# Optimization experiments

Measured on AMD Instinct MI355X. Metric: run time of the kernel, lower is better.

Reference implementation:

```python
import jax, jax.numpy as jnp
import numpy as np

N_GRID = 65160   # 181*360 lat-lon grid nodes (= self.size)
N_MESH = 40962   # level-6 icosphere nodes
N_TOT = N_GRID + N_MESH
E = 521280
IN_CH = 96
HID = 256
OUT_CH = 96


def setup_inputs() -> dict:
    key = jax.random.key(0)
    ks = jax.random.split(key, 12)
    inp = {
        'x': jax.random.normal(ks[0], (1, IN_CH, N_MESH), jnp.float32),
        'x_res_grid': jax.random.normal(ks[1], (1, IN_CH, N_GRID), jnp.float32),
        'edge_index': jax.random.randint(ks[2], (2, E), 0, N_TOT, jnp.int64),
        # GCNConv 1 (in_ch -> 256), glorot-ish scale
        'W1': jax.random.normal(ks[3], (IN_CH, HID), jnp.float32) * (2.0 / (IN_CH + HID)) ** 0.5,
        'b1': jnp.zeros((HID,), jnp.float32),
        # GCNConv 2 (256 -> 256)
        'W2': jax.random.normal(ks[4], (HID, HID), jnp.float32) * (2.0 / (HID + HID)) ** 0.5,
        'b2': jnp.zeros((HID,), jnp.float32),
        # Lmodel2: Linear(256,256) -> Linear(256,out_ch), xavier_normal
        'Wl1': jax.random.normal(ks[5], (HID, HID), jnp.float32) * (2.0 / (HID + HID)) ** 0.5,
        'bl1': jnp.zeros((HID,), jnp.float32),
        'Wl2': jax.random.normal(ks[6], (HID, OUT_CH), jnp.float32) * (2.0 / (HID + OUT_CH)) ** 0.5,
        'bl2': jnp.zeros((OUT_CH,), jnp.float32),
    }
    return inp


def _gcn_norm(edge_index, n_nodes):
    # PyG gcn_norm with add_self_loops=True, edge_weight=1
    loop = jnp.arange(n_nodes, dtype=edge_index.dtype)
    src = jnp.concatenate([edge_index[0], loop])
    dst = jnp.concatenate([edge_index[1], loop])
    deg = jnp.zeros((n_nodes,), jnp.float32).at[dst].add(1.0)
    dinv = jnp.where(deg > 0, jax.lax.rsqrt(deg), 0.0)
    norm = dinv[src] * dinv[dst]  # [E+N]
    return src, dst, norm


def _gcn_conv(h, W, b, src, dst, norm):
    # h: [B, N, C] -> [B, N, H]; x' = D^-1/2 (A+I) D^-1/2 (h W) + b
    m = h @ W                                   # [B, N, H]
    msg = m[:, src, :] * norm[None, :, None]    # [B, E+N, H]
    agg = jnp.zeros(m.shape, m.dtype).at[:, dst].add(msg)
    return agg + b


def reference(x, x_res_grid, edge_index, W1, b1, W2, b2, Wl1, bl1, Wl2, bl2):
    nodes = jnp.concatenate([x_res_grid, x], axis=-1)  # [B, C, N]
    h = nodes.transpose(0, 2, 1)                       # [B, N, C]
    n = h.shape[1]
    src, dst, norm = _gcn_norm(edge_index, n)
    h = _gcn_conv(h, W1, b1, src, dst, norm)
    h = jax.nn.gelu(h, approximate=False)              # torch nn.GELU (exact erf)
    h = _gcn_conv(h, W2, b2, src, dst, norm)           # [B, N, 256]
    g = h[:, :N_GRID, :]                               # slice grid nodes
    out = (g @ Wl1 + bl1) @ Wl2 + bl2                  # [B, size, out_ch]
    return out.transpose(0, 2, 1)                      # [B, out_ch, size]
```

## Files before the change

### kernel.cpp

```cpp
#include <hip/hip_runtime.h>
#include <math.h>

#define N_GRID 65160
#define N_MESH 40962
#define N_TOT  106122
#define NE     521280
#define IN_CH  96
#define HID    256
#define OUT_CH 96

typedef __attribute__((ext_vector_type(8))) short bf16x8;
typedef __attribute__((ext_vector_type(4))) float f32x4;

__device__ __forceinline__ unsigned short f2bf(float f) {
  unsigned u = __float_as_uint(f);
  return (unsigned short)((u + 0x7FFFu + ((u >> 16) & 1u)) >> 16);
}
__device__ __forceinline__ float bf2f(unsigned short s) {
  return __uint_as_float(((unsigned)s) << 16);
}
__device__ __forceinline__ float4 ldbf4(const unsigned short* p) {
  ushort4 u = *(const ushort4*)p;
  return make_float4(bf2f(u.x), bf2f(u.y), bf2f(u.z), bf2f(u.w));
}

__global__ void k_concat_transpose(const float* __restrict__ xg, const float* __restrict__ xm,
                                   unsigned short* __restrict__ h) {
  __shared__ float tile[IN_CH][65];
  int base = blockIdx.x * 64;
  int t = threadIdx.x;
#pragma unroll
  for (int it = 0; it < 24; ++it) {
    int lin = t + it * 256;
    int c  = lin >> 6;
    int n0 = lin & 63;
    int n = base + n0;
    float v = 0.f;
    if (n < N_TOT) {
      v = (n < N_GRID) ? xg[(size_t)c * N_GRID + n]
                       : xm[(size_t)c * N_MESH + (n - N_GRID)];
    }
    tile[c][n0] = v;
  }
  __syncthreads();
#pragma unroll
  for (int it = 0; it < 24; ++it) {
    int lin = t + it * 256;
    int c  = lin % 96;
    int n0 = lin / 96;
    int n = base + n0;
    if (n < N_TOT) h[(size_t)n * IN_CH + c] = f2bf(tile[c][n0]);
  }
}

__global__ void k_transpose_out(const float* __restrict__ tb, float* __restrict__ out) {
  __shared__ float tile[IN_CH][65];
  int base = blockIdx.x * 64;
  int t = threadIdx.x;
#pragma unroll
  for (int it = 0; it < 24; ++it) {
    int lin = t + it * 256;
    int c  = lin % 96;
    int n0 = lin / 96;
    int n = base + n0;
    if (n < N_GRID) tile[c][n0] = tb[(size_t)n * 96 + c];
  }
  __syncthreads();
#pragma unroll
  for (int it = 0; it < 24; ++it) {
    int lin = t + it * 256;
    int c  = lin >> 6;
    int n0 = lin & 63;
    int n = base + n0;
    if (n < N_GRID) out[(size_t)c * N_GRID + n] = tile[c][n0];
  }
}

__global__ void k_zeroi(int* __restrict__ p, int n) {
  int i = blockIdx.x * 256 + threadIdx.x;
  if (i < n) p[i] = 0;
}
__global__ void k_seti(int* __restrict__ p, int v) { *p = v; }

__global__ void k_hist(const int* __restrict__ dst, int* __restrict__ deg) {
  int e = blockIdx.x * 256 + threadIdx.x;
  if (e < NE) atomicAdd(&deg[dst[e]], 1);
}

__global__ void k_blocksum(const int* __restrict__ deg, int* __restrict__ bsum, int n) {
  __shared__ int s[256];
  int i = blockIdx.x * 256 + threadIdx.x;
  s[threadIdx.x] = (i < n) ? deg[i] : 0;
  __syncthreads();
  for (int st = 128; st > 0; st >>= 1) {
    if (threadIdx.x < st) s[threadIdx.x] += s[threadIdx.x + st];
    __syncthreads();
  }
  if (threadIdx.x == 0) bsum[blockIdx.x] = s[0];
}

__global__ void k_scanbsum(int* __restrict__ bsum, int nb) {
  __shared__ int s[512];
  int t = threadIdx.x;
  int v = (t < nb) ? bsum[t] : 0;
  s[t] = v;
  __syncthreads();
  for (int off = 1; off < 512; off <<= 1) {
    int x = (t >= off) ? s[t - off] : 0;
    __syncthreads();
    s[t] += x;
    __syncthreads();
  }
  if (t < nb) bsum[t] = s[t] - v;
}

__global__ void k_offsets(const int* __restrict__ deg, const int* __restrict__ bsum,
                          int* __restrict__ off, int* __restrict__ cur, int n) {
  __shared__ int s[256];
  int i = blockIdx.x * 256 + threadIdx.x;
  int v = (i < n) ? deg[i] : 0;
  s[threadIdx.x] = v;
  __syncthreads();
  for (int o = 1; o < 256; o <<= 1) {
    int x = (threadIdx.x >= o) ? s[threadIdx.x - o] : 0;
    __syncthreads();
    s[threadIdx.x] += x;
    __syncthreads();
  }
  if (i < n) {
    int e = bsum[blockIdx.x] + s[threadIdx.x] - v;
    off[i] = e;
    cur[i] = e;
  }
}

__global__ void k_fillcsr(const int* __restrict__ src, const int* __restrict__ dst,
                          int* __restrict__ cur, int* __restrict__ csrc) {
  int e = blockIdx.x * 256 + threadIdx.x;
  if (e < NE) {
    int p = atomicAdd(&cur[dst[e]], 1);
    csrc[p] = src[e];
  }
}

__global__ void k_dinv(const int* __restrict__ deg, float* __restrict__ dinv, int n) {
  int i = blockIdx.x * 256 + threadIdx.x;
  if (i < n) dinv[i] = rsqrtf(1.0f + (float)deg[i]);
}

__global__ void k_gather96(const int* __restrict__ off, const int* __restrict__ csrc,
                           const float* __restrict__ dinv, const unsigned short* __restrict__ h,
                           unsigned short* __restrict__ agg) {
  int i = blockIdx.x * 256 + threadIdx.x;
  if (i >= N_TOT * 24) return;
  int n = i / 24;
  int c4 = (i % 24) << 2;
  float di = dinv[n];
  float4 v = ldbf4(h + (size_t)n * 96 + c4);
  float w0 = di * di;
  float4 acc = make_float4(v.x * w0, v.y * w0, v.z * w0, v.w * w0);
  int e0 = off[n], e1 = off[n + 1];
  int e = e0;
  for (; e + 3 < e1; e += 4) {
    int s0 = csrc[e], s1 = csrc[e + 1], s2 = csrc[e + 2], s3 = csrc[e + 3];
    float wa = dinv[s0] * di, wb = dinv[s1] * di, wc = dinv[s2] * di, wd = dinv[s3] * di;
    float4 u0 = ldbf4(h + (size_t)s0 * 96 + c4);
    float4 u1 = ldbf4(h + (size_t)s1 * 96 + c4);
    float4 u2 = ldbf4(h + (size_t)s2 * 96 + c4);
    float4 u3 = ldbf4(h + (size_t)s3 * 96 + c4);
    acc.x += u0.x * wa + u1.x * wb + u2.x * wc + u3.x * wd;
    acc.y += u0.y * wa + u1.y * wb + u2.y * wc + u3.y * wd;
    acc.z += u0.z * wa + u1.z * wb + u2.z * wc + u3.z * wd;
    acc.w += u0.w * wa + u1.w * wb + u2.w * wc + u3.w * wd;
  }
  for (; e < e1; ++e) {
    int s = csrc[e];
    float w = dinv[s] * di;
    float4 u = ldbf4(h + (size_t)s * 96 + c4);
    acc.x += u.x * w; acc.y += u.y * w; acc.z += u.z * w; acc.w += u.w * w;
  }
  ushort4 o;
  o.x = f2bf(acc.x); o.y = f2bf(acc.y); o.z = f2bf(acc.z); o.w = f2bf(acc.w);
  *(ushort4*)(agg + (size_t)n * 96 + c4) = o;
}

__global__ void k_gather96p(const int* __restrict__ off, const int* __restrict__ csrc,
                            const float* __restrict__ dinv, const unsigned short* __restrict__ p,
                            const float* __restrict__ bc, float* __restrict__ tb) {
  int i = blockIdx.x * 256 + threadIdx.x;
  if (i >= N_GRID * 24) return;
  int n = i / 24;
  int c4 = (i % 24) << 2;
  float di = dinv[n];
  float4 v = ldbf4(p + (size_t)n * 96 + c4);
  float w0 = di * di;
  float4 acc = make_float4(v.x * w0, v.y * w0, v.z * w0, v.w * w0);
  int e0 = off[n], e1 = off[n + 1];
  int e = e0;
  for (; e + 3 < e1; e += 4) {
    int s0 = csrc[e], s1 = csrc[e + 1], s2 = csrc[e + 2], s3 = csrc[e + 3];
    float wa = dinv[s0] * di, wb = dinv[s1] * di, wc = dinv[s2] * di, wd = dinv[s3] * di;
    float4 u0 = ldbf4(p + (size_t)s0 * 96 + c4);
    float4 u1 = ldbf4(p + (size_t)s1 * 96 + c4);
    float4 u2 = ldbf4(p + (size_t)s2 * 96 + c4);
    float4 u3 = ldbf4(p + (size_t)s3 * 96 + c4);
    acc.x += u0.x * wa + u1.x * wb + u2.x * wc + u3.x * wd;
    acc.y += u0.y * wa + u1.y * wb + u2.y * wc + u3.y * wd;
    acc.z += u0.z * wa + u1.z * wb + u2.z * wc + u3.z * wd;
    acc.w += u0.w * wa + u1.w * wb + u2.w * wc + u3.w * wd;
  }
  for (; e < e1; ++e) {
    int s = csrc[e];
    float w = dinv[s] * di;
    float4 u = ldbf4(p + (size_t)s * 96 + c4);
    acc.x += u.x * w; acc.y += u.y * w; acc.z += u.z * w; acc.w += u.w * w;
  }
  float4 b = *(const float4*)(bc + c4);
  acc.x += b.x; acc.y += b.y; acc.z += b.z; acc.w += b.w;
  *(float4*)(tb + (size_t)n * 96 + c4) = acc;
}

__global__ __launch_bounds__(256, 2) void k_wgemm96(const float* __restrict__ A, const float* __restrict__ bvec,
                                                    const float* __restrict__ B, float* __restrict__ C,
                                                    int M, int K) {
  __shared__ float As[64][33];
  __shared__ float Bs[64][100];
  int t = threadIdx.x;
  int tx = t & 15, ty = t >> 4;
  int bm = blockIdx.x * 32;
  float acc[2][6] = {};
  for (int kc = 0; kc < K; kc += 64) {
#pragma unroll
    for (int it = 0; it < 2; ++it) {
      int idx = t + it * 256;
      int r = idx >> 4, k4 = (idx & 15) << 2;
      int gr = bm + r;
      float4 v = make_float4(0.f, 0.f, 0.f, 0.f);
      if (gr < M) {
        const float* src = (gr < M - 1) ? (A + (size_t)gr * K + kc + k4) : (bvec + kc + k4);
        v = *(const float4*)src;
      }
      As[k4 + 0][r] = v.x;
      As[k4 + 1][r] = v.y;
      As[k4 + 2][r] = v.z;
      As[k4 + 3][r] = v.w;
    }
#pragma unroll
    for (int it = 0; it < 6; ++it) {
      int idx = t + it * 256;
      int k = idx / 24, j4 = (idx % 24) << 2;
      float4 v = *(const float4*)(B + (size_t)(kc + k) * 96 + j4);
      *(float4*)&Bs[k][j4] = v;
    }
    __syncthreads();
#pragma unroll
    for (int k = 0; k < 64; ++k) {
      float a0 = As[k][ty * 2], a1 = As[k][ty * 2 + 1];
      float w[6];
      *(float2*)&w[0] = *(const float2*)&Bs[k][tx * 6];
      *(float2*)&w[2] = *(const float2*)&Bs[k][tx * 6 + 2];
      *(float2*)&w[4] = *(const float2*)&Bs[k][tx * 6 + 4];
#pragma unroll
      for (int j = 0; j < 6; ++j) { acc[0][j] += a0 * w[j]; acc[1][j] += a1 * w[j]; }
    }
    __syncthreads();
  }
#pragma unroll
  for (int i = 0; i < 2; ++i) {
    int gr = bm + ty * 2 + i;
    if (gr >= M) continue;
    float* row = C + (size_t)gr * 96 + tx * 6;
    row[0] = acc[i][0]; row[1] = acc[i][1]; row[2] = acc[i][2];
    row[3] = acc[i][3]; row[4] = acc[i][4]; row[5] = acc[i][5];
  }
}

__global__ void k_bc_final(const float* __restrict__ r1, const float* __restrict__ r2,
                           const float* __restrict__ bl2, float* __restrict__ bc) {
  int j = threadIdx.x;
  if (j < OUT_CH) bc[j] = r1[j] + r2[j] + bl2[j];
}

__global__ void k_cast_w1t(const float* __restrict__ W1, unsigned short* __restrict__ W1bt) {
  int idx = blockIdx.x * 256 + threadIdx.x;
  if (idx >= 256 * 96) return;
  int n = idx / 96, k = idx % 96;
  W1bt[idx] = f2bf(W1[(size_t)k * 256 + n]);
}
__global__ void k_cast_wct(const float* __restrict__ Wc, unsigned short* __restrict__ Wcbt) {
  int idx = blockIdx.x * 256 + threadIdx.x;
  if (idx >= 96 * 256) return;
  int n = idx / 256, k = idx % 256;
  Wcbt[idx] = f2bf(Wc[(size_t)k * 96 + n]);
}

__global__ __launch_bounds__(256, 2) void k_mlp(const unsigned short* __restrict__ A,
                                                const unsigned short* __restrict__ W1bt,
                                                const float* __restrict__ bias1,
                                                const unsigned short* __restrict__ Wcbt,
                                                unsigned short* __restrict__ P, int M) {
  __shared__ unsigned short As[64][104];
  __shared__ unsigned short Hs[64][264];
  __shared__ unsigned short Ws[6656];
  int t = threadIdx.x;
  int wave = t >> 6, lane = t & 63;
  int l15 = lane & 15, lhi = lane >> 4;
  int bm = blockIdx.x * 64;

#pragma unroll
  for (int it = 0; it < 3; ++it) {
    int idx = t + it * 256;
    int row = idx / 12, g = idx % 12;
    uint4 v = make_uint4(0u, 0u, 0u, 0u);
    if (bm + row < M) v = *(const uint4*)(A + (size_t)(bm + row) * 96 + g * 8);
    *(uint4*)&As[row][g * 8] = v;
  }
  __syncthreads();

  int arow = wave * 16 + l15;
  bf16x8 a0 = *(const bf16x8*)&As[arow][0  + lhi * 8];
  bf16x8 a1 = *(const bf16x8*)&As[arow][32 + lhi * 8];
  bf16x8 a2 = *(const bf16x8*)&As[arow][64 + lhi * 8];
  int hrow = wave * 16 + lhi * 4;

  for (int c = 0; c < 4; ++c) {
    __syncthreads();
#pragma unroll
    for (int it = 0; it < 3; ++it) {
      int idx = t + it * 256;
      int row = idx / 12, g = idx % 12;
      *(uint4*)&Ws[row * 104 + g * 8] = *(const uint4*)(W1bt + (size_t)(c * 64 + row) * 96 + g * 8);
    }
    __syncthreads();
#pragma unroll
    for (int fl = 0; fl < 4; ++fl) {
      int f = c * 4 + fl;
      const unsigned short* wp = &Ws[(fl * 16 + l15) * 104 + lhi * 8];
      bf16x8 w0_ = *(const bf16x8*)(wp);
      bf16x8 w1_ = *(const bf16x8*)(wp + 32);
      bf16x8 w2_ = *(const bf16x8*)(wp + 64);
      f32x4 acc = (f32x4){0.f, 0.f, 0.f, 0.f};
      acc = __builtin_amdgcn_mfma_f32_16x16x32_bf16(a0, w0_, acc, 0, 0, 0);
      acc = __builtin_amdgcn_mfma_f32_16x16x32_bf16(a1, w1_, acc, 0, 0, 0);
      acc = __builtin_amdgcn_mfma_f32_16x16x32_bf16(a2, w2_, acc, 0, 0, 0);
      int col = f * 16 + l15;
      float bv = bias1[col];
#pragma unroll
      for (int r = 0; r < 4; ++r) {
        float x = acc[r] + bv;
        x = 0.5f * x * (1.0f + erff(x * 0.70710678118654752f));
        Hs[hrow + r][col] = f2bf(x);
      }
    }
  }

  int orow = wave * 16 + lhi * 4;
  for (int tf = 0; tf < 2; ++tf) {
    f32x4 accC[3];
#pragma unroll
    for (int fl = 0; fl < 3; ++fl) accC[fl] = (f32x4){0.f, 0.f, 0.f, 0.f};
    for (int kh = 0; kh < 2; ++kh) {
      __syncthreads();
#pragma unroll
      for (int it = 0; it < 3; ++it) {
        int idx = t + it * 256;
        int row = idx >> 4, g = idx & 15;
        *(uint4*)&Ws[row * 136 + g * 8] =
            *(const uint4*)(Wcbt + (size_t)(tf * 48 + row) * 256 + kh * 128 + g * 8);
      }
      __syncthreads();
#pragma unroll
      for (int fl = 0; fl < 3; ++fl) {
        const unsigned short* wp = &Ws[(fl * 16 + l15) * 136 + lhi * 8];
#pragma unroll
        for (int ks = 0; ks < 4; ++ks) {
          bf16x8 av = *(const bf16x8*)&Hs[wave * 16 + l15][(kh * 4 + ks) * 32 + lhi * 8];
          bf16x8 wv = *(const bf16x8*)(wp + ks * 32);
          accC[fl] = __builtin_amdgcn_mfma_f32_16x16x32_bf16(av, wv, accC[fl], 0, 0, 0);
        }
      }
    }
#pragma unroll
    for (int fl = 0; fl < 3; ++fl) {
      int col = (tf * 3 + fl) * 16 + l15;
#pragma unroll
      for (int r = 0; r < 4; ++r) As[orow + r][col] = f2bf(accC[fl][r]);
    }
  }
  __syncthreads();
#pragma unroll
  for (int it = 0; it < 3; ++it) {
    int idx = t + it * 256;
    int row = idx / 12, g = idx % 12;
    if (bm + row < M) *(uint4*)(P + (size_t)(bm + row) * 96 + g * 8) = *(const uint4*)&As[row][g * 8];
  }
}

extern "C" void kernel_launch(void* const* d_in, const int* in_sizes, int n_in,
                              void* d_out, int out_size, void* d_ws, size_t ws_size,
                              hipStream_t stream) {
  const float* xm  = (const float*)d_in[0];
  const float* xg  = (const float*)d_in[1];
  const int*   ei  = (const int*)d_in[2];
  const float* W1  = (const float*)d_in[3];
  const float* b1  = (const float*)d_in[4];
  const float* W2  = (const float*)d_in[5];
  const float* b2  = (const float*)d_in[6];
  const float* Wl1 = (const float*)d_in[7];
  const float* bl1 = (const float*)d_in[8];
  const float* Wl2 = (const float*)d_in[9];
  const float* bl2 = (const float*)d_in[10];
  float* out = (float*)d_out;

  float* W0 = (float*)d_ws;
  const size_t MB = (size_t)N_GRID * 256;
  int*   deg  = (int*)(W0 + MB);
  int*   off  = deg + N_TOT;
  int*   cur  = off + N_TOT + 1;
  int*   bsum = cur + N_TOT;
  int*   csrc = bsum + 512;
  float* dinv = (float*)(csrc + NE);
  size_t p1off = ((size_t)(dinv + N_TOT - W0) + 3) & ~(size_t)3;
  float* P1 = W0 + p1off;
  float* P2 = P1 + 257 * 96;
  float* bc = P2 + 257 * 96;
  size_t wboff = ((size_t)(bc + 96 - W0) + 3) & ~(size_t)3;
  unsigned short* W1bt = (unsigned short*)(W0 + wboff);
  unsigned short* Wcbt = W1bt + 256 * 96;
  size_t RH = (wboff + 24576 + 3) & ~(size_t)3;
  unsigned short* hb = (unsigned short*)(W0 + RH);
  unsigned short* agg1b = (unsigned short*)W0;
  unsigned short* p = (unsigned short*)(hb + (size_t)N_TOT * 96 + 16);
  p = (unsigned short*)(((size_t)p + 15) & ~(size_t)15);
  float* tb = W0 + (size_t)6 * 1024 * 1024;

  const int* esrc = ei;
  const int* edst = ei + NE;
  dim3 b256(256);
  const int NB_N = (N_TOT + 255) / 256;

  k_concat_transpose<<<dim3((N_TOT + 63) / 64), b256, 0, stream>>>(xg, xm, hb);

  k_zeroi<<<dim3(NB_N), b256, 0, stream>>>(deg, N_TOT);
  k_hist<<<dim3((NE + 255) / 256), b256, 0, stream>>>(edst, deg);
  k_blocksum<<<dim3(NB_N), b256, 0, stream>>>(deg, bsum, N_TOT);
  k_scanbsum<<<dim3(1), dim3(512), 0, stream>>>(bsum, NB_N);
  k_offsets<<<dim3(NB_N), b256, 0, stream>>>(deg, bsum, off, cur, N_TOT);
  k_seti<<<dim3(1), dim3(1), 0, stream>>>(off + N_TOT, NE);
  k_fillcsr<<<dim3((NE + 255) / 256), b256, 0, stream>>>(esrc, edst, cur, csrc);
  k_dinv<<<dim3(NB_N), b256, 0, stream>>>(deg, dinv, N_TOT);
  k_cast_w1t<<<dim3(96), b256, 0, stream>>>(W1, W1bt);
  k_wgemm96<<<dim3(9), b256, 0, stream>>>(Wl1, bl1, Wl2, P1, 257, HID);
  k_wgemm96<<<dim3(9), b256, 0, stream>>>(W2, b2, P1, P2, 257, HID);
  k_bc_final<<<dim3(1), dim3(96), 0, stream>>>(P1 + 256 * 96, P2 + 256 * 96, bl2, bc);
  k_cast_wct<<<dim3(96), b256, 0, stream>>>(P2, Wcbt);

  k_gather96<<<dim3((N_TOT * 24 + 255) / 256), b256, 0, stream>>>(off, csrc, dinv, hb, agg1b);

  k_mlp<<<dim3((N_TOT + 63) / 64), b256, 0, stream>>>(agg1b, W1bt, b1, Wcbt, p, N_TOT);

  k_gather96p<<<dim3((N_GRID * 24 + 255) / 256), b256, 0, stream>>>(off, csrc, dinv, p, bc, tb);

  k_transpose_out<<<dim3((N_GRID + 63) / 64), b256, 0, stream>>>(tb, out);
}
```

Before: 249.0 us.

## Swizzle MLP shared-memory tiles and drop A/output staging buffers

Replaces the padded shared-memory layouts of the weight and hidden tiles in the fused MLP kernel with XOR-swizzled layouts, so MFMA operand loads avoid bank conflicts without padding. The A operand is now loaded straight from global memory into registers instead of being staged through shared memory. Output is written directly from the accumulators rather than through a shared-memory staging tile. Together these reduce shared-memory footprint and barriers, which may raise occupancy. The trade-off is that the direct output writes become uncoalesced 2-byte scattered stores instead of 16-byte rows.

```diff
diff --git a/kernel.cpp b/kernel.cpp
--- a/kernel.cpp
+++ b/kernel.cpp
@@ -294,33 +294,26 @@
   Wcbt[idx] = f2bf(Wc[(size_t)k * 96 + n]);
 }
 
+#define SWZ(row, g) (((row) << 7) + (((g) ^ ((row) & 7)) << 3))
+#define SWZH(row, g) (((row) << 8) + (((g) ^ ((row) & 7)) << 3))
 __global__ __launch_bounds__(256, 2) void k_mlp(const unsigned short* __restrict__ A,
                                                 const unsigned short* __restrict__ W1bt,
                                                 const float* __restrict__ bias1,
                                                 const unsigned short* __restrict__ Wcbt,
                                                 unsigned short* __restrict__ P, int M) {
-  __shared__ unsigned short As[64][104];
-  __shared__ unsigned short Hs[64][264];
-  __shared__ unsigned short Ws[6656];
+  __shared__ unsigned short Hs[64 * 256];
+  __shared__ unsigned short Ws[64 * 128];
   int t = threadIdx.x;
   int wave = t >> 6, lane = t & 63;
   int l15 = lane & 15, lhi = lane >> 4;
   int bm = blockIdx.x * 64;
 
-#pragma unroll
-  for (int it = 0; it < 3; ++it) {
-    int idx = t + it * 256;
-    int row = idx / 12, g = idx % 12;
-    uint4 v = make_uint4(0u, 0u, 0u, 0u);
-    if (bm + row < M) v = *(const uint4*)(A + (size_t)(bm + row) * 96 + g * 8);
-    *(uint4*)&As[row][g * 8] = v;
-  }
-  __syncthreads();
-
-  int arow = wave * 16 + l15;
-  bf16x8 a0 = *(const bf16x8*)&As[arow][0  + lhi * 8];
-  bf16x8 a1 = *(const bf16x8*)&As[arow][32 + lhi * 8];
-  bf16x8 a2 = *(const bf16x8*)&As[arow][64 + lhi * 8];
+  int arowl = wave * 16 + l15;
+  bool aok = (bm + arowl) < M;
+  const unsigned short* ap = A + (size_t)(bm + arowl) * 96 + lhi * 8;
+  bf16x8 a0 = aok ? *(const bf16x8*)(ap)      : (bf16x8){0,0,0,0,0,0,0,0};
+  bf16x8 a1 = aok ? *(const bf16x8*)(ap + 32) : (bf16x8){0,0,0,0,0,0,0,0};
+  bf16x8 a2 = aok ? *(const bf16x8*)(ap + 64) : (bf16x8){0,0,0,0,0,0,0,0};
   int hrow = wave * 16 + lhi * 4;
 
   for (int c = 0; c < 4; ++c) {
@@ -329,16 +322,16 @@
     for (int it = 0; it < 3; ++it) {
       int idx = t + it * 256;
       int row = idx / 12, g = idx % 12;
-      *(uint4*)&Ws[row * 104 + g * 8] = *(const uint4*)(W1bt + (size_t)(c * 64 + row) * 96 + g * 8);
+      *(uint4*)&Ws[SWZ(row, g)] = *(const uint4*)(W1bt + (size_t)(c * 64 + row) * 96 + g * 8);
     }
     __syncthreads();
 #pragma unroll
     for (int fl = 0; fl < 4; ++fl) {
       int f = c * 4 + fl;
-      const unsigned short* wp = &Ws[(fl * 16 + l15) * 104 + lhi * 8];
-      bf16x8 w0_ = *(const bf16x8*)(wp);
-      bf16x8 w1_ = *(const bf16x8*)(wp + 32);
-      bf16x8 w2_ = *(const bf16x8*)(wp + 64);
+      int wrow = fl * 16 + l15;
+      bf16x8 w0_ = *(const bf16x8*)&Ws[SWZ(wrow, 0 + lhi)];
+      bf16x8 w1_ = *(const bf16x8*)&Ws[SWZ(wrow, 4 + lhi)];
+      bf16x8 w2_ = *(const bf16x8*)&Ws[SWZ(wrow, 8 + lhi)];
       f32x4 acc = (f32x4){0.f, 0.f, 0.f, 0.f};
       acc = __builtin_amdgcn_mfma_f32_16x16x32_bf16(a0, w0_, acc, 0, 0, 0);
       acc = __builtin_amdgcn_mfma_f32_16x16x32_bf16(a1, w1_, acc, 0, 0, 0);
@@ -349,7 +342,8 @@
       for (int r = 0; r < 4; ++r) {
         float x = acc[r] + bv;
         x = 0.5f * x * (1.0f + erff(x * 0.70710678118654752f));
-        Hs[hrow + r][col] = f2bf(x);
+        int row = hrow + r;
+        Hs[SWZH(row, col >> 3) + (col & 7)] = f2bf(x);
       }
     }
   }
@@ -365,17 +359,18 @@
       for (int it = 0; it < 3; ++it) {
         int idx = t + it * 256;
         int row = idx >> 4, g = idx & 15;
-        *(uint4*)&Ws[row * 136 + g * 8] =
+        *(uint4*)&Ws[SWZ(row, g)] =
             *(const uint4*)(Wcbt + (size_t)(tf * 48 + row) * 256 + kh * 128 + g * 8);
       }
       __syncthreads();
 #pragma unroll
       for (int fl = 0; fl < 3; ++fl) {
-        const unsigned short* wp = &Ws[(fl * 16 + l15) * 136 + lhi * 8];
+        int wrow = fl * 16 + l15;
+        int harow = wave * 16 + l15;
 #pragma unroll
         for (int ks = 0; ks < 4; ++ks) {
-          bf16x8 av = *(const bf16x8*)&Hs[wave * 16 + l15][(kh * 4 + ks) * 32 + lhi * 8];
-          bf16x8 wv = *(const bf16x8*)(wp + ks * 32);
+          bf16x8 av = *(const bf16x8*)&Hs[SWZH(harow, (kh * 4 + ks) * 4 + lhi)];
+          bf16x8 wv = *(const bf16x8*)&Ws[SWZ(wrow, ks * 4 + lhi)];
           accC[fl] = __builtin_amdgcn_mfma_f32_16x16x32_bf16(av, wv, accC[fl], 0, 0, 0);
         }
       }
@@ -384,15 +379,11 @@
     for (int fl = 0; fl < 3; ++fl) {
       int col = (tf * 3 + fl) * 16 + l15;
 #pragma unroll
-      for (int r = 0; r < 4; ++r) As[orow + r][col] = f2bf(accC[fl][r]);
-    }
-  }
-  __syncthreads();
-#pragma unroll
-  for (int it = 0; it < 3; ++it) {
-    int idx = t + it * 256;
-    int row = idx / 12, g = idx % 12;
-    if (bm + row < M) *(uint4*)(P + (size_t)(bm + row) * 96 + g * 8) = *(const uint4*)&As[row][g * 8];
+      for (int r = 0; r < 4; ++r) {
+        int row = bm + orow + r;
+        if (row < M) P[(size_t)row * 96 + col] = f2bf(accC[fl][r]);
+      }
+    }
   }
 }
 
```

Result: faster. 239.3 us (-3.9%).
